# Performance work log

Measured on AMD Instinct MI355X. Metric: run time of the kernel, lower is better.

Reference implementation:

```python
import jax, jax.numpy as jnp
import numpy as np

B, T, D, H, L = 128, 512, 512, 512, 2

def setup_inputs() -> dict:
    key = jax.random.key(0)
    k1, k2 = jax.random.split(key)
    x = jax.random.normal(k1, (B, T, D), dtype=jnp.float32)
    hiddens = jnp.zeros((L, 2, B, H), dtype=jnp.float32)  # [layer, (h,c), batch, hidden]
    # stacked per-layer fused-gate weights; torch Linear(in+hid, 4*hid)
    W = jax.random.normal(k2, (L, D + H, 4 * H), dtype=jnp.float32) * (1.0 / np.sqrt(D + H))
    b = jnp.zeros((L, 4 * H), dtype=jnp.float32)
    return {"x": x, "hiddens": hiddens, "W": W, "b": b}

def reference(x, hiddens, W, b):
    num_layers = W.shape[0]

    def step(hid, x_t):
        inp = x_t
        new = []
        for l in range(num_layers):
            h, c = hid[l, 0], hid[l, 1]
            gates = jnp.concatenate([inp, h], axis=-1) @ W[l] + b[l]  # [B, 4H]
            i, f, g, o = jnp.split(gates, 4, axis=-1)
            i = jax.nn.sigmoid(i)
            f = jax.nn.sigmoid(f)
            g = jnp.tanh(g)
            o = jax.nn.sigmoid(o)
            c_t = f * c + i * g
            h_t = o * jnp.tanh(c_t)
            new.append(jnp.stack([h_t, c_t], axis=0))
            inp = h_t
        hid = jnp.stack(new, axis=0)
        return hid, inp  # emit top-layer h per timestep

    hiddens_final, outs = jax.lax.scan(step, hiddens, jnp.swapaxes(x, 0, 1))
    outputs = jnp.swapaxes(outs, 0, 1)  # [B, T, H]
    return outputs, hiddens_final
```

## Files before the change

### kernel.cpp

```cpp
#include <hip/hip_runtime.h>
#include <stdint.h>

typedef __attribute__((ext_vector_type(4))) int   i32x4;
typedef __attribute__((ext_vector_type(8))) short bf16x8;
typedef __attribute__((ext_vector_type(4))) float f32x4;

#define DEV static __device__ __forceinline__

constexpr int  kB = 128, kT = 512, kD = 512, kH = 512;
constexpr int  kGC = 2048;
constexpr int  ROWS = 32;
constexpr int  NG = 4;
constexpr int  NJ = 32;
constexpr int  NTHREADS = 512;
constexpr size_t SLOT_ELEMS = (size_t)kB * kH;
constexpr size_t WIMG_ELEMS = (size_t)2 * NJ * 4 * 32 * 512;
constexpr size_t WIMG_BYTES = WIMG_ELEMS * 2;
constexpr int  RFULL = kT + 1;

DEV ushort f2bf(float f) {
  uint32_t u = __float_as_uint(f);
  u += 0x7fff + ((u >> 16) & 1);
  return (ushort)(u >> 16);
}
DEV int pk2(float a, float b) { return (int)((uint32_t)f2bf(a) | ((uint32_t)f2bf(b) << 16)); }
DEV float sigf(float v)  { return 1.f / (1.f + __expf(-v)); }
DEV float tanhf_(float v){ return 1.f - 2.f / (__expf(2.f * v) + 1.f); }

__global__ void prep_w(const float* __restrict__ W, ushort* __restrict__ wimg) {
  uint32_t idx = blockIdx.x * 256u + threadIdx.x;
  int e = idx & 7, lane = (idx >> 3) & 63, ks = (idx >> 9) & 31;
  int G = (idx >> 14) & 3, j = (idx >> 16) & 31, l = (idx >> 21) & 1;
  int k = ks * 32 + ((lane >> 4) << 3) + e;
  int c = G * 512 + j * 16 + (lane & 15);
  wimg[idx] = f2bf(W[(size_t)l * 1024 * 2048 + (size_t)k * 2048 + c]);
}

__global__ void prep_init(const float* __restrict__ hiddens, ushort* __restrict__ r0, ushort* __restrict__ r1) {
  uint32_t idx = blockIdx.x * 256u + threadIdx.x;
  int l = idx >> 16; uint32_t r = idx & 65535u;
  ushort v = f2bf(hiddens[(size_t)(l * 2 + 0) * 65536 + r]);
  (l ? r1 : r0)[r] = v;
}

template<bool BIG>
DEV void stage_ring(ushort* Abuf_, const ushort* rbase, int g, int tid) {
  #pragma unroll
  for (int p = 0; p < 4; ++p) {
    int o = (tid + p * NTHREADS) * 16;
    int row = o >> 10, kb = o & 1023;
    const ushort* src = rbase + (size_t)(g * ROWS + row) * kH + (kb >> 1);
    i32x4 v;
    if (BIG) {
      v = *reinterpret_cast<const i32x4*>(src);
    } else {
      uint64_t lo = __hip_atomic_load((const uint64_t*)src,       __ATOMIC_RELAXED, __HIP_MEMORY_SCOPE_AGENT);
      uint64_t hi = __hip_atomic_load((const uint64_t*)(src + 4), __ATOMIC_RELAXED, __HIP_MEMORY_SCOPE_AGENT);
      v[0] = (int)(uint32_t)lo; v[1] = (int)(uint32_t)(lo >> 32);
      v[2] = (int)(uint32_t)hi; v[3] = (int)(uint32_t)(hi >> 32);
    }
    *reinterpret_cast<i32x4*>(reinterpret_cast<char*>(Abuf_) + ((row * 1024 + kb) ^ ((row & 7) << 4))) = v;
  }
}

template<bool BIG>
__launch_bounds__(NTHREADS, 2)
__global__ void lstm_main(const float* __restrict__ x, const float* __restrict__ hiddens,
                          const float* __restrict__ bias, const ushort* __restrict__ wimg,
                          ushort* __restrict__ ring0, ushort* __restrict__ ring1,
                          int* __restrict__ cnt, int* __restrict__ cons0,
                          float* __restrict__ out, int R0, int R1) {
  __shared__ ushort Abuf[ROWS * 512];
  __shared__ float  gbuf[4][ROWS][16];
  __shared__ float  cbuf[ROWS][16];
  __shared__ float  hbuf[ROWS][16];

  const int tid  = threadIdx.x;
  const int lane = tid & 63;
  const int wv   = tid >> 6;
  const int G    = wv & 3;
  const int rf   = wv >> 2;
  const int j    = blockIdx.x & 31;
  const int g    = (blockIdx.x >> 5) & 3;
  const int l    = blockIdx.x >> 7;

  __threadfence();

  i32x4 wr[32];
  {
    const ushort* base = wimg + (((size_t)(l * NJ + j) * 4 + G) * 32) * 512 + lane * 8;
    #pragma unroll
    for (int ks = 0; ks < 32; ++ks)
      wr[ks] = *reinterpret_cast<const i32x4*>(base + ks * 512);
  }
  const float bval = bias[l * kGC + G * 512 + j * 16 + (lane & 15)];
  {
    int row = tid >> 4, col = tid & 15;
    cbuf[row][col] = hiddens[((size_t)(l * 2 + 1) * kB + (g * ROWS + row)) * kH + j * 16 + col];
  }
  int* mycnt = cnt + (l * NG + g) * kT;
  int* c0cnt = cnt + g * kT;
  ushort* rrec = l ? ring1 : ring0;
  const int Rrec = l ? R1 : R0;

  const int arow  = rf * 16 + (lane & 15);
  const int koff  = (lane >> 4) << 3;
  const int abase = arow * 1024;
  const int aswz  = (arow & 7) << 4;

  __syncthreads();

  for (int t = 0; t < kT; ++t) {
    if (l == 1) {
      if (tid == 0) {
        while (__hip_atomic_load(&c0cnt[t], __ATOMIC_RELAXED, __HIP_MEMORY_SCOPE_AGENT) < NJ)
          __builtin_amdgcn_s_sleep(2);
      }
      __syncthreads();
      stage_ring<BIG>(Abuf, ring0 + (size_t)((t + 1) % R0) * SLOT_ELEMS, g, tid);
    } else {
      #pragma unroll
      for (int p = 0; p < 4; ++p) {
        int o = (tid + p * NTHREADS) * 16;
        int row = o >> 10, kb = o & 1023;
        const float* src = x + ((size_t)(g * ROWS + row) * kT + t) * kD + (kb >> 1);
        f32x4 f0 = *reinterpret_cast<const f32x4*>(src);
        f32x4 f1 = *reinterpret_cast<const f32x4*>(src + 4);
        i32x4 v;
        v[0] = pk2(f0[0], f0[1]); v[1] = pk2(f0[2], f0[3]);
        v[2] = pk2(f1[0], f1[1]); v[3] = pk2(f1[2], f1[3]);
        *reinterpret_cast<i32x4*>(reinterpret_cast<char*>(Abuf) + ((row * 1024 + kb) ^ ((row & 7) << 4))) = v;
      }
    }
    __syncthreads();
    if (!BIG && l == 1 && tid == 0)
      __hip_atomic_fetch_add(&cons0[g * kT + t], 1, __ATOMIC_RELAXED, __HIP_MEMORY_SCOPE_AGENT);

    f32x4 acc = {};
    #pragma unroll
    for (int ks = 0; ks < 16; ++ks) {
      int off = (abase + ((ks * 32 + koff) << 1)) ^ aswz;
      i32x4 av = *reinterpret_cast<const i32x4*>(reinterpret_cast<const char*>(Abuf) + off);
      acc = __builtin_amdgcn_mfma_f32_16x16x32_bf16(
              *reinterpret_cast<bf16x8*>(&av), *reinterpret_cast<bf16x8*>(&wr[ks]), acc, 0, 0, 0);
    }
    __syncthreads();

    if (t > 0) {
      if (tid == 0) {
        while (__hip_atomic_load(&mycnt[t - 1], __ATOMIC_RELAXED, __HIP_MEMORY_SCOPE_AGENT) < NJ)
          __builtin_amdgcn_s_sleep(2);
        if (!BIG && l == 0 && t >= R0) {
          while (__hip_atomic_load(&cons0[g * kT + (t - R0)], __ATOMIC_RELAXED, __HIP_MEMORY_SCOPE_AGENT) < NJ)
            __builtin_amdgcn_s_sleep(2);
        }
      }
      __syncthreads();
    }
    stage_ring<BIG>(Abuf, rrec + (size_t)(t % Rrec) * SLOT_ELEMS, g, tid);
    __syncthreads();

    #pragma unroll
    for (int ks = 0; ks < 16; ++ks) {
      int off = (abase + ((ks * 32 + koff) << 1)) ^ aswz;
      i32x4 av = *reinterpret_cast<const i32x4*>(reinterpret_cast<const char*>(Abuf) + off);
      acc = __builtin_amdgcn_mfma_f32_16x16x32_bf16(
              *reinterpret_cast<bf16x8*>(&av), *reinterpret_cast<bf16x8*>(&wr[16 + ks]), acc, 0, 0, 0);
    }

    #pragma unroll
    for (int q = 0; q < 4; ++q) {
      float v2 = acc[q] + bval;
      v2 = (G == 2) ? tanhf_(v2) : sigf(v2);
      gbuf[G][rf * 16 + ((lane >> 4) << 2) + q][lane & 15] = v2;
    }
    __syncthreads();

    {
      int row = tid >> 4, col = tid & 15;
      float iv = gbuf[0][row][col], fv = gbuf[1][row][col];
      float gv = gbuf[2][row][col], ov = gbuf[3][row][col];
      float cc = fv * cbuf[row][col] + iv * gv;
      cbuf[row][col] = cc;
      float hh = ov * tanhf_(cc);
      hbuf[row][col] = hh;
      int b = g * ROWS + row;
      if (l == 1) out[((size_t)b * kT + t) * kH + j * 16 + col] = hh;
      if (t == kT - 1) {
        size_t hb = (size_t)kB * kT * kH;
        out[hb + ((size_t)(l * 2 + 0) * kB + b) * kH + j * 16 + col] = hh;
        out[hb + ((size_t)(l * 2 + 1) * kB + b) * kH + j * 16 + col] = cc;
      }
    }
    __syncthreads();

    if (tid < 256) {
      int row = tid >> 3, cp = tid & 7;
      uint32_t pkv = (uint32_t)f2bf(hbuf[row][2 * cp]) | ((uint32_t)f2bf(hbuf[row][2 * cp + 1]) << 16);
      uint32_t* dst = (uint32_t*)(rrec + (size_t)((t + 1) % Rrec) * SLOT_ELEMS
                                  + (size_t)(g * ROWS + row) * kH + j * 16 + 2 * cp);
      __hip_atomic_store(dst, pkv, __ATOMIC_RELAXED, __HIP_MEMORY_SCOPE_AGENT);
    }
    asm volatile("s_waitcnt vmcnt(0)" ::: "memory");
    __syncthreads();
    if (tid == 0)
      __hip_atomic_fetch_add(&mycnt[t], 1, __ATOMIC_RELAXED, __HIP_MEMORY_SCOPE_AGENT);
  }
}

extern "C" void kernel_launch(void* const* d_in, const int* in_sizes, int n_in,
                              void* d_out, int out_size, void* d_ws, size_t ws_size,
                              hipStream_t stream) {
  const float* x  = (const float*)d_in[0];
  const float* hd = (const float*)d_in[1];
  const float* W  = (const float*)d_in[2];
  const float* b  = (const float*)d_in[3];
  float* out = (float*)d_out;

  char* ws = (char*)d_ws;
  ushort* wimg = (ushort*)ws;
  int* cnt  = (int*)(ws + WIMG_BYTES);
  int* cons = (int*)(ws + WIMG_BYTES + 16384);
  size_t ringoff = WIMG_BYTES + 32768;
  size_t avail = ws_size > ringoff ? ws_size - ringoff : 0;
  long rmax = (long)(avail / (2 * SLOT_ELEMS * 2));
  int R = (rmax >= RFULL) ? RFULL : (rmax >= 16 ? 16 : (rmax >= 2 ? (int)rmax : 2));
  ushort* ring0 = (ushort*)(ws + ringoff);
  ushort* ring1 = ring0 + (size_t)R * SLOT_ELEMS;

  hipMemsetAsync(ws + WIMG_BYTES, 0, 32768, stream);
  prep_w<<<(int)(WIMG_ELEMS / 256), 256, 0, stream>>>(W, wimg);
  prep_init<<<(2 * kB * kH) / 256, 256, 0, stream>>>(hd, ring0, ring1);
  if (R == RFULL)
    lstm_main<true ><<<256, NTHREADS, 0, stream>>>(x, hd, b, wimg, ring0, ring1, cnt, cons, out, R, R);
  else
    lstm_main<false><<<256, NTHREADS, 0, stream>>>(x, hd, b, wimg, ring0, ring1, cnt, cons, out, R, R);
}
```

Baseline: 2.120 ms.

## Replace counter-based inter-block sync with canary-polled data ring for full-ring path

Adds an lstm_big kernel used when the workspace holds the full timestep ring. Instead of separate counters and barriers, blocks poll the ring slots directly and spin until the canary value (0x7F7F7F7F) written by a memset is overwritten by the producer's atomic store. This fuses the sync signal with the data load and drops the counter traffic. In exchange it memsets the whole ring each call and relies on bf16 results never matching the canary pattern, plus relaxed-ordering visibility of each packed word.

```diff
diff --git a/kernel.cpp b/kernel.cpp
--- a/kernel.cpp
+++ b/kernel.cpp
@@ -17,6 +17,7 @@
 constexpr size_t WIMG_ELEMS = (size_t)2 * NJ * 4 * 32 * 512;
 constexpr size_t WIMG_BYTES = WIMG_ELEMS * 2;
 constexpr int  RFULL = kT + 1;
+constexpr uint32_t CANARY = 0x7F7F7F7Fu;
 
 DEV ushort f2bf(float f) {
   uint32_t u = __float_as_uint(f);
@@ -26,6 +27,13 @@
 DEV int pk2(float a, float b) { return (int)((uint32_t)f2bf(a) | ((uint32_t)f2bf(b) << 16)); }
 DEV float sigf(float v)  { return 1.f / (1.f + __expf(-v)); }
 DEV float tanhf_(float v){ return 1.f - 2.f / (__expf(2.f * v) + 1.f); }
+
+DEV uint64_t ald64(const uint64_t* p) {
+  return __hip_atomic_load(p, __ATOMIC_RELAXED, __HIP_MEMORY_SCOPE_AGENT);
+}
+DEV bool bad64(uint64_t v) {
+  return ((uint32_t)v == CANARY) || ((uint32_t)(v >> 32) == CANARY);
+}
 
 __global__ void prep_w(const float* __restrict__ W, ushort* __restrict__ wimg) {
   uint32_t idx = blockIdx.x * 256u + threadIdx.x;
@@ -42,6 +50,148 @@
   ushort v = f2bf(hiddens[(size_t)(l * 2 + 0) * 65536 + r]);
   (l ? r1 : r0)[r] = v;
 }
+
+
+struct Poll { uint64_t d[8]; };
+
+DEV void poll_issue(Poll& P, const ushort* sb, int g, int tid) {
+  #pragma unroll
+  for (int p = 0; p < 4; ++p) {
+    int o = (tid + p * NTHREADS) * 16, row = o >> 10, kb = o & 1023;
+    const uint64_t* s = reinterpret_cast<const uint64_t*>(sb + (size_t)(g * ROWS + row) * kH + (kb >> 1));
+    P.d[2 * p]     = ald64(s);
+    P.d[2 * p + 1] = ald64(s + 1);
+  }
+}
+
+template<int SLP>
+DEV void poll_finish(Poll& P, const ushort* sb, ushort* Ab, int g, int tid) {
+  #pragma unroll
+  for (int p = 0; p < 4; ++p) {
+    int o = (tid + p * NTHREADS) * 16, row = o >> 10, kb = o & 1023;
+    const uint64_t* s = reinterpret_cast<const uint64_t*>(sb + (size_t)(g * ROWS + row) * kH + (kb >> 1));
+    uint64_t lo = P.d[2 * p], hi = P.d[2 * p + 1];
+    while (bad64(lo) || bad64(hi)) {
+      __builtin_amdgcn_s_sleep(SLP);
+      lo = ald64(s); hi = ald64(s + 1);
+    }
+    i32x4 v;
+    v[0] = (int)(uint32_t)lo; v[1] = (int)(uint32_t)(lo >> 32);
+    v[2] = (int)(uint32_t)hi; v[3] = (int)(uint32_t)(hi >> 32);
+    *reinterpret_cast<i32x4*>(reinterpret_cast<char*>(Ab) + ((row * 1024 + kb) ^ ((row & 7) << 4))) = v;
+  }
+}
+
+__launch_bounds__(NTHREADS, 2)
+__global__ void lstm_big(const float* __restrict__ x, const float* __restrict__ hiddens,
+                         const float* __restrict__ bias, const ushort* __restrict__ wimg,
+                         ushort* __restrict__ ring0, ushort* __restrict__ ring1,
+                         float* __restrict__ out) {
+  __shared__ ushort AbufX[ROWS * 512];
+  __shared__ ushort AbufH[ROWS * 512];
+  __shared__ float  gbuf[4][ROWS][16];
+
+  const int tid  = threadIdx.x;
+  const int lane = tid & 63;
+  const int wv   = tid >> 6;
+  const int G    = wv & 3;
+  const int rf   = wv >> 2;
+  const int j    = blockIdx.x & 31;
+  const int g    = (blockIdx.x >> 5) & 3;
+  const int l    = blockIdx.x >> 7;
+
+  __threadfence();
+
+  i32x4 wr[32];
+  {
+    const ushort* base = wimg + (((size_t)(l * NJ + j) * 4 + G) * 32) * 512 + lane * 8;
+    #pragma unroll
+    for (int ks = 0; ks < 32; ++ks)
+      wr[ks] = *reinterpret_cast<const i32x4*>(base + ks * 512);
+  }
+  const float bval = bias[l * kGC + G * 512 + j * 16 + (lane & 15)];
+  const int urow = tid >> 4, ucol = tid & 15;
+  float creg = hiddens[((size_t)(l * 2 + 1) * kB + (g * ROWS + urow)) * kH + j * 16 + ucol];
+
+  ushort* rrec = l ? ring1 : ring0;
+
+  const int arow  = rf * 16 + (lane & 15);
+  const int koff  = (lane >> 4) << 3;
+  const int abase = arow * 1024;
+  const int aswz  = (arow & 7) << 4;
+
+  for (int t = 0; t < kT; ++t) {
+    Poll hp, xp;
+    const ushort* hsrc = rrec + (size_t)t * SLOT_ELEMS;
+    poll_issue(hp, hsrc, g, tid);
+    const ushort* xsrc = ring0 + (size_t)(t + 1) * SLOT_ELEMS;
+    if (l == 1) {
+      poll_issue(xp, xsrc, g, tid);
+    } else {
+      #pragma unroll
+      for (int p = 0; p < 4; ++p) {
+        int o = (tid + p * NTHREADS) * 16, row = o >> 10, kb = o & 1023;
+        const float* src = x + ((size_t)(g * ROWS + row) * kT + t) * kD + (kb >> 1);
+        f32x4 f0 = *reinterpret_cast<const f32x4*>(src);
+        f32x4 f1 = *reinterpret_cast<const f32x4*>(src + 4);
+        i32x4 v;
+        v[0] = pk2(f0[0], f0[1]); v[1] = pk2(f0[2], f0[3]);
+        v[2] = pk2(f1[0], f1[1]); v[3] = pk2(f1[2], f1[3]);
+        *reinterpret_cast<i32x4*>(reinterpret_cast<char*>(AbufX) + ((row * 1024 + kb) ^ ((row & 7) << 4))) = v;
+      }
+    }
+    poll_finish<1>(hp, hsrc, AbufH, g, tid);
+    if (l == 1) poll_finish<4>(xp, xsrc, AbufX, g, tid);
+    __syncthreads();
+
+    f32x4 acc = {};
+    #pragma unroll
+    for (int ks = 0; ks < 16; ++ks) {
+      int off = (abase + ((ks * 32 + koff) << 1)) ^ aswz;
+      i32x4 av = *reinterpret_cast<const i32x4*>(reinterpret_cast<const char*>(AbufX) + off);
+      acc = __builtin_amdgcn_mfma_f32_16x16x32_bf16(
+              *reinterpret_cast<bf16x8*>(&av), *reinterpret_cast<bf16x8*>(&wr[ks]), acc, 0, 0, 0);
+    }
+    #pragma unroll
+    for (int ks = 0; ks < 16; ++ks) {
+      int off = (abase + ((ks * 32 + koff) << 1)) ^ aswz;
+      i32x4 av = *reinterpret_cast<const i32x4*>(reinterpret_cast<const char*>(AbufH) + off);
+      acc = __builtin_amdgcn_mfma_f32_16x16x32_bf16(
+              *reinterpret_cast<bf16x8*>(&av), *reinterpret_cast<bf16x8*>(&wr[16 + ks]), acc, 0, 0, 0);
+    }
+
+    #pragma unroll
+    for (int q = 0; q < 4; ++q) {
+      float v2 = acc[q] + bval;
+      v2 = (G == 2) ? tanhf_(v2) : sigf(v2);
+      gbuf[G][rf * 16 + ((lane >> 4) << 2) + q][lane & 15] = v2;
+    }
+    __syncthreads();
+
+    {
+      float iv = gbuf[0][urow][ucol], fv = gbuf[1][urow][ucol];
+      float gv = gbuf[2][urow][ucol], ov = gbuf[3][urow][ucol];
+      creg = fv * creg + iv * gv;
+      float hh = ov * tanhf_(creg);
+      int b = g * ROWS + urow;
+      uint32_t me    = f2bf(hh);
+      uint32_t other = (uint32_t)__shfl_xor((int)me, 1);
+      if (!(ucol & 1)) {
+        uint32_t pkv = me | (other << 16);
+        uint32_t* dst = (uint32_t*)(rrec + (size_t)(t + 1) * SLOT_ELEMS
+                                    + (size_t)b * kH + j * 16 + ucol);
+        __hip_atomic_store(dst, pkv, __ATOMIC_RELAXED, __HIP_MEMORY_SCOPE_AGENT);
+      }
+      if (l == 1) out[((size_t)b * kT + t) * kH + j * 16 + ucol] = hh;
+      if (t == kT - 1) {
+        size_t hb = (size_t)kB * kT * kH;
+        out[hb + ((size_t)(l * 2 + 0) * kB + b) * kH + j * 16 + ucol] = hh;
+        out[hb + ((size_t)(l * 2 + 1) * kB + b) * kH + j * 16 + ucol] = creg;
+      }
+    }
+  }
+}
+
 
 template<bool BIG>
 DEV void stage_ring(ushort* Abuf_, const ushort* rbase, int g, int tid) {
@@ -228,11 +378,15 @@
   ushort* ring0 = (ushort*)(ws + ringoff);
   ushort* ring1 = ring0 + (size_t)R * SLOT_ELEMS;
 
-  hipMemsetAsync(ws + WIMG_BYTES, 0, 32768, stream);
-  prep_w<<<(int)(WIMG_ELEMS / 256), 256, 0, stream>>>(W, wimg);
-  prep_init<<<(2 * kB * kH) / 256, 256, 0, stream>>>(hd, ring0, ring1);
-  if (R == RFULL)
-    lstm_main<true ><<<256, NTHREADS, 0, stream>>>(x, hd, b, wimg, ring0, ring1, cnt, cons, out, R, R);
-  else
+  if (R == RFULL) {
+    hipMemsetAsync(ring0, 0x7F, (size_t)2 * RFULL * SLOT_ELEMS * 2, stream);
+    prep_w<<<(int)(WIMG_ELEMS / 256), 256, 0, stream>>>(W, wimg);
+    prep_init<<<(2 * kB * kH) / 256, 256, 0, stream>>>(hd, ring0, ring1);
+    lstm_big<<<256, NTHREADS, 0, stream>>>(x, hd, b, wimg, ring0, ring1, out);
+  } else {
+    hipMemsetAsync(ws + WIMG_BYTES, 0, 32768, stream);
+    prep_w<<<(int)(WIMG_ELEMS / 256), 256, 0, stream>>>(W, wimg);
+    prep_init<<<(2 * kB * kH) / 256, 256, 0, stream>>>(hd, ring0, ring1);
     lstm_main<false><<<256, NTHREADS, 0, stream>>>(x, hd, b, wimg, ring0, ring1, cnt, cons, out, R, R);
-}
+  }
+}
```

After: 3.181 ms. +50.1%, slower.
